# Kernel optimization log

Measured on AMD Instinct MI355X. Metric: run time of the kernel, lower is better.

The kernel has to match this reference:

```python
import jax, jax.numpy as jnp
import numpy as np

N_NODES, N_EDGES = 100000, 1600000
D_IN, D_H, D_OUT = 256, 128, 32


def _gcn_conv(x, W, b, row, col, norm, n):
    # GCNConv: transform, normalized gather from source nodes, scatter-sum at targets, bias.
    h = x @ W                                   # [n, d_out]
    msgs = h[row] * norm[:, None]               # [E', d_out] edge messages
    out = jax.ops.segment_sum(msgs, col, num_segments=n)
    return out + b


def setup_inputs() -> dict:
    key = jax.random.key(0)
    k = jax.random.split(key, 6)
    x = jax.random.normal(k[0], (N_NODES, D_IN), dtype=jnp.float32)
    edge_index = jax.random.randint(k[1], (2, N_EDGES), 0, N_NODES, dtype=jnp.int64)
    # Glorot-ish scaled params (GCNConv lin has no bias; bias added post-aggregation)
    W1 = jax.random.normal(k[2], (D_IN, D_H), dtype=jnp.float32) * (1.0 / np.sqrt(D_IN))
    b1 = jnp.zeros((D_H,), dtype=jnp.float32)
    W2 = jax.random.normal(k[3], (D_H, D_OUT), dtype=jnp.float32) * (1.0 / np.sqrt(D_H))
    b2 = jnp.zeros((D_OUT,), dtype=jnp.float32)
    return {"x": x, "W1": W1, "b1": b1, "W2": W2, "b2": b2, "edge_index": edge_index}


def reference(x, W1, b1, W2, b2, edge_index):
    n = x.shape[0]
    loops = jnp.arange(n, dtype=edge_index.dtype)
    row = jnp.concatenate([edge_index[0], loops])   # sources (incl. self-loops)
    col = jnp.concatenate([edge_index[1], loops])   # targets
    # symmetric normalization deg^{-1/2} (deg >= 1 because of self-loops)
    deg = jax.ops.segment_sum(jnp.ones_like(col, dtype=x.dtype), col, num_segments=n)
    dinv = deg ** -0.5
    norm = dinv[row] * dinv[col]
    h = jax.nn.relu(_gcn_conv(x, W1, b1, row, col, norm, n))
    # F.dropout(training=False) is identity in eval mode
    out = _gcn_conv(h, W2, b2, row, col, norm, n)
    return jax.nn.log_softmax(out, axis=1)
```

## Files before the change

kernel.cpp:

```cpp
#include <hip/hip_runtime.h>
#include <math.h>

#define N_NODES 100000
#define N_EDGES 1600000
#define D_IN 256
#define D_H 128
#define D_OUT 32
#define N_PAD 102400
#define NB 196
#define CAPB 10240
#define CHUNK 2048

typedef long long ll;
typedef unsigned int uint;
typedef unsigned short ushort;
typedef unsigned char uchar;
typedef short frag_ab __attribute__((ext_vector_type(8)));
typedef float frag_cd __attribute__((ext_vector_type(4)));

__device__ __forceinline__ ushort f2bf(float f) {
    uint u = __float_as_uint(f);
    u += 0x7FFFu + ((u >> 16) & 1u);
    return (ushort)(u >> 16);
}
__device__ __forceinline__ float bfl(uint u) { return __uint_as_float(u << 16); }
__device__ __forceinline__ float bfh(uint u) { return __uint_as_float(u & 0xFFFF0000u); }
__device__ __forceinline__ uint packbf(float a, float b) {
    return (uint)f2bf(a) | ((uint)f2bf(b) << 16);
}

__global__ __launch_bounds__(256) void k_bucketA(const int* __restrict__ row,
                                                 const int* __restrict__ col,
                                                 int* __restrict__ deg,
                                                 int* __restrict__ gcur,
                                                 uint* __restrict__ pairs,
                                                 const float* __restrict__ W1,
                                                 const float* __restrict__ W2,
                                                 ushort* __restrict__ w1t,
                                                 ushort* __restrict__ w2t, int e) {
    __shared__ int cnt[NB];
    __shared__ int lofs[NB];
    __shared__ int lstart[NB];
    __shared__ int sc[256];
    __shared__ uint spair[CHUNK];
    __shared__ uchar sbuck[CHUNK];
    const int t = threadIdx.x;
    for (int i = t; i < NB; i += 256) cnt[i] = 0;
    __syncthreads();
    const int base = blockIdx.x * CHUNK;
    const int end = min(base + CHUNK, e);
    const int valid = end - base;
    for (int idx = base + t; idx < end; idx += 256) {
        int c = col[idx];
        atomicAdd(&deg[c], 1);
        atomicAdd(&cnt[c >> 9], 1);
    }
    __syncthreads();
    int v = (t < NB) ? cnt[t] : 0;
    sc[t] = v;
    __syncthreads();
    for (int o = 1; o < 256; o <<= 1) {
        int u2 = (t >= o) ? sc[t - o] : 0;
        __syncthreads();
        sc[t] += u2;
        __syncthreads();
    }
    if (t < NB) {
        lofs[t] = sc[t] - v;
        lstart[t] = (v > 0) ? atomicAdd(&gcur[t], v) : 0;
        cnt[t] = 0;
    }
    __syncthreads();
    for (int idx = base + t; idx < end; idx += 256) {
        int c = col[idx], r = row[idx];
        int b = c >> 9;
        int pos = lofs[b] + atomicAdd(&cnt[b], 1);
        spair[pos] = ((uint)r << 9) | (uint)(c & 511);
        sbuck[pos] = (uchar)b;
    }
    __syncthreads();
    for (int i = t; i < valid; i += 256) {
        int b = sbuck[i];
        int rel = lstart[b] + (i - lofs[b]);
        if (rel < CAPB) pairs[b * CAPB + rel] = spair[i];
    }
    int gi = blockIdx.x * 256 + t;
    if (gi < D_IN * D_H) {
        int k = gi >> 7, nn = gi & 127;
        w1t[nn * D_IN + k] = f2bf(W1[gi]);
    } else if (gi < D_IN * D_H + D_H * D_OUT) {
        int j = gi - D_IN * D_H;
        int k = j >> 5, nn = j & 31;
        w2t[nn * D_H + k] = f2bf(W2[j]);
    }
}

__global__ __launch_bounds__(256) void k_fillB(const uint* __restrict__ pairs,
                                               const int* __restrict__ gcur,
                                               const int* __restrict__ deg,
                                               int* __restrict__ rp,
                                               float* __restrict__ dinv,
                                               int* __restrict__ csr_src, int n) {
    __shared__ int scsr[CAPB];
    __shared__ int lrp[512];
    __shared__ int cur[512];
    __shared__ int ssum[256];
    const int b = blockIdx.x, t = threadIdx.x;
    const int node0 = b << 9;
    int d0 = deg[node0 + 2 * t];
    int d1 = deg[node0 + 2 * t + 1];
    ssum[t] = d0 + d1;
    __syncthreads();
    for (int o = 1; o < 256; o <<= 1) {
        int u2 = (t >= o) ? ssum[t - o] : 0;
        __syncthreads();
        ssum[t] += u2;
        __syncthreads();
    }
    int excl = ssum[t] - (d0 + d1);
    lrp[2 * t] = excl;
    lrp[2 * t + 1] = excl + d0;
    cur[2 * t] = excl;
    cur[2 * t + 1] = excl + d0;
    __syncthreads();
    for (int i = t; i < 512; i += 256) {
        int vv = node0 + i;
        if (vv < n) {
            rp[vv] = b * CAPB + lrp[i];
            dinv[vv] = rsqrtf((float)(1 + deg[vv]));
        }
    }
    const int cnt = min(gcur[b], CAPB);
    const uint* pr = pairs + b * CAPB;
    for (int i = t; i < cnt; i += 256) {
        uint pp = pr[i];
        int pos = atomicAdd(&cur[pp & 511], 1);
        if (pos < CAPB) scsr[pos] = (int)(pp >> 9);
    }
    __syncthreads();
    for (int i = t; i < cnt; i += 256)
        csr_src[b * CAPB + i] = scsr[i];
}

__global__ __launch_bounds__(256, 3) void k_gemm1(const float* __restrict__ x,
                                                  const ushort* __restrict__ w1t,
                                                  const float* __restrict__ dinv,
                                                  ushort* __restrict__ hxs, int n) {
    const int tid = threadIdx.x;
    const int wv = tid >> 6, lane = tid & 63;
    const int lm = lane & 15, quad = lane >> 4;
    const int base = blockIdx.x * 128 + wv * 32;

    frag_cd acc[2][8];
#pragma unroll
    for (int mt = 0; mt < 2; mt++)
#pragma unroll
        for (int nt = 0; nt < 8; nt++) acc[mt][nt] = (frag_cd){0.f, 0.f, 0.f, 0.f};

    const float4* xr[2];
#pragma unroll
    for (int mt = 0; mt < 2; mt++) {
        int node = base + mt * 16 + lm;
        xr[mt] = (const float4*)(x + (ll)min(node, n - 1) * D_IN);
    }

#pragma unroll
    for (int ks = 0; ks < 8; ks++) {
        frag_ab a[2];
#pragma unroll
        for (int mt = 0; mt < 2; mt++) {
            float4 v0 = xr[mt][ks * 8 + quad * 2];
            float4 v1 = xr[mt][ks * 8 + quad * 2 + 1];
            uint* ap = (uint*)&a[mt];
            ap[0] = packbf(v0.x, v0.y);
            ap[1] = packbf(v0.z, v0.w);
            ap[2] = packbf(v1.x, v1.y);
            ap[3] = packbf(v1.z, v1.w);
        }
#pragma unroll
        for (int nt = 0; nt < 8; nt++) {
            frag_ab b = *(const frag_ab*)&w1t[(nt * 16 + lm) * D_IN + ks * 32 + quad * 8];
#pragma unroll
            for (int mt = 0; mt < 2; mt++)
                acc[mt][nt] = __builtin_amdgcn_mfma_f32_16x16x32_bf16(
                    a[mt], b, acc[mt][nt], 0, 0, 0);
        }
    }

#pragma unroll
    for (int mt = 0; mt < 2; mt++) {
#pragma unroll
        for (int r = 0; r < 4; r++) {
            int node = base + mt * 16 + quad * 4 + r;
            if (node < n) {
                float dv = dinv[node];
#pragma unroll
                for (int nt = 0; nt < 8; nt++)
                    hxs[(ll)node * D_H + nt * 16 + lm] = f2bf(acc[mt][nt][r] * dv);
            }
        }
    }
}

__global__ __launch_bounds__(256) void k_agg1(const uint* __restrict__ hxs,
                                              const int* __restrict__ csr_src,
                                              const int* __restrict__ rp,
                                              const int* __restrict__ deg,
                                              const float* __restrict__ dinv,
                                              const float* __restrict__ b1,
                                              uint* __restrict__ h, int n) {
    int v = blockIdx.x * 4 + (threadIdx.x >> 6);
    if (v >= n) return;
    int lane = threadIdx.x & 63;
    uint u = hxs[v * 64 + lane];
    float a0 = bfl(u), a1 = bfh(u);
    int s = rp[v], e = s + deg[v];
    int i = s;
    for (; i + 7 < e; i += 8) {
        int s0 = csr_src[i], s1 = csr_src[i + 1];
        int s2 = csr_src[i + 2], s3 = csr_src[i + 3];
        int s4 = csr_src[i + 4], s5 = csr_src[i + 5];
        int s6 = csr_src[i + 6], s7 = csr_src[i + 7];
        uint u0 = hxs[s0 * 64 + lane], u1 = hxs[s1 * 64 + lane];
        uint u2 = hxs[s2 * 64 + lane], u3 = hxs[s3 * 64 + lane];
        uint u4 = hxs[s4 * 64 + lane], u5 = hxs[s5 * 64 + lane];
        uint u6 = hxs[s6 * 64 + lane], u7 = hxs[s7 * 64 + lane];
        a0 += bfl(u0) + bfl(u1) + bfl(u2) + bfl(u3) + bfl(u4) + bfl(u5) + bfl(u6) + bfl(u7);
        a1 += bfh(u0) + bfh(u1) + bfh(u2) + bfh(u3) + bfh(u4) + bfh(u5) + bfh(u6) + bfh(u7);
    }
    for (; i + 1 < e; i += 2) {
        int s0 = csr_src[i], s1 = csr_src[i + 1];
        uint u0 = hxs[s0 * 64 + lane], u1 = hxs[s1 * 64 + lane];
        a0 += bfl(u0) + bfl(u1);
        a1 += bfh(u0) + bfh(u1);
    }
    if (i < e) {
        uint u0 = hxs[csr_src[i] * 64 + lane];
        a0 += bfl(u0);
        a1 += bfh(u0);
    }
    float dv = dinv[v];
    float2 bb = ((const float2*)b1)[lane];
    h[v * 64 + lane] = packbf(fmaxf(fmaf(dv, a0, bb.x), 0.f),
                              fmaxf(fmaf(dv, a1, bb.y), 0.f));
}

__global__ __launch_bounds__(256) void k_gemm2(const ushort* __restrict__ h,
                                               const ushort* __restrict__ w2t,
                                               const float* __restrict__ dinv,
                                               ushort* __restrict__ hx2s, int n) {
    const int tid = threadIdx.x;
    const int wv = tid >> 6, lane = tid & 63;
    const int lm = lane & 15, quad = lane >> 4;
    const int base = blockIdx.x * 128 + wv * 32;

    frag_cd acc[2][2];
#pragma unroll
    for (int mt = 0; mt < 2; mt++)
#pragma unroll
        for (int nt = 0; nt < 2; nt++) acc[mt][nt] = (frag_cd){0.f, 0.f, 0.f, 0.f};

    const ushort* hr[2];
#pragma unroll
    for (int mt = 0; mt < 2; mt++) {
        int node = base + mt * 16 + lm;
        hr[mt] = h + (ll)min(node, n - 1) * D_H;
    }

#pragma unroll
    for (int ks = 0; ks < 4; ks++) {
        frag_ab a[2], b[2];
#pragma unroll
        for (int mt = 0; mt < 2; mt++)
            a[mt] = *(const frag_ab*)&hr[mt][ks * 32 + quad * 8];
#pragma unroll
        for (int nt = 0; nt < 2; nt++)
            b[nt] = *(const frag_ab*)&w2t[(nt * 16 + lm) * D_H + ks * 32 + quad * 8];
#pragma unroll
        for (int mt = 0; mt < 2; mt++)
#pragma unroll
            for (int nt = 0; nt < 2; nt++)
                acc[mt][nt] = __builtin_amdgcn_mfma_f32_16x16x32_bf16(
                    a[mt], b[nt], acc[mt][nt], 0, 0, 0);
    }

#pragma unroll
    for (int mt = 0; mt < 2; mt++) {
#pragma unroll
        for (int r = 0; r < 4; r++) {
            int node = base + mt * 16 + quad * 4 + r;
            if (node < n) {
                float dv = dinv[node];
#pragma unroll
                for (int nt = 0; nt < 2; nt++)
                    hx2s[(ll)node * D_OUT + nt * 16 + lm] = f2bf(acc[mt][nt][r] * dv);
            }
        }
    }
}

__global__ __launch_bounds__(256) void k_agg2(const uint* __restrict__ hx2s,
                                              const int* __restrict__ csr_src,
                                              const int* __restrict__ rp,
                                              const int* __restrict__ deg,
                                              const float* __restrict__ dinv,
                                              const float* __restrict__ b2,
                                              float2* __restrict__ out, int n) {
    int v = blockIdx.x * 16 + (threadIdx.x >> 4);
    if (v >= n) return;
    int l16 = threadIdx.x & 15;
    uint u = hx2s[v * 16 + l16];
    float a0 = bfl(u), a1 = bfh(u);
    int s = rp[v], e = s + deg[v];
    int i = s;
    for (; i + 7 < e; i += 8) {
        int s0 = csr_src[i], s1 = csr_src[i + 1];
        int s2 = csr_src[i + 2], s3 = csr_src[i + 3];
        int s4 = csr_src[i + 4], s5 = csr_src[i + 5];
        int s6 = csr_src[i + 6], s7 = csr_src[i + 7];
        uint u0 = hx2s[s0 * 16 + l16], u1 = hx2s[s1 * 16 + l16];
        uint u2 = hx2s[s2 * 16 + l16], u3 = hx2s[s3 * 16 + l16];
        uint u4 = hx2s[s4 * 16 + l16], u5 = hx2s[s5 * 16 + l16];
        uint u6 = hx2s[s6 * 16 + l16], u7 = hx2s[s7 * 16 + l16];
        a0 += bfl(u0) + bfl(u1) + bfl(u2) + bfl(u3) + bfl(u4) + bfl(u5) + bfl(u6) + bfl(u7);
        a1 += bfh(u0) + bfh(u1) + bfh(u2) + bfh(u3) + bfh(u4) + bfh(u5) + bfh(u6) + bfh(u7);
    }
    for (; i + 1 < e; i += 2) {
        int s0 = csr_src[i], s1 = csr_src[i + 1];
        uint u0 = hx2s[s0 * 16 + l16], u1 = hx2s[s1 * 16 + l16];
        a0 += bfl(u0) + bfl(u1);
        a1 += bfh(u0) + bfh(u1);
    }
    if (i < e) {
        uint u0 = hx2s[csr_src[i] * 16 + l16];
        a0 += bfl(u0);
        a1 += bfh(u0);
    }
    float dv = dinv[v];
    float2 bb = ((const float2*)b2)[l16];
    float t0 = fmaf(dv, a0, bb.x), t1 = fmaf(dv, a1, bb.y);
    float mx = fmaxf(t0, t1);
#pragma unroll
    for (int m = 8; m >= 1; m >>= 1) mx = fmaxf(mx, __shfl_xor(mx, m));
    float sum = __expf(t0 - mx) + __expf(t1 - mx);
#pragma unroll
    for (int m = 8; m >= 1; m >>= 1) sum += __shfl_xor(sum, m);
    float lse = mx + __logf(sum);
    out[v * 16 + l16] = make_float2(t0 - lse, t1 - lse);
}

extern "C" void kernel_launch(void* const* d_in, const int* in_sizes, int n_in,
                              void* d_out, int out_size, void* d_ws, size_t ws_size,
                              hipStream_t stream) {
    const float* x  = (const float*)d_in[0];
    const float* W1 = (const float*)d_in[1];
    const float* b1 = (const float*)d_in[2];
    const float* W2 = (const float*)d_in[3];
    const float* b2 = (const float*)d_in[4];
    const int*   ei = (const int*)d_in[5];
    const int* row = ei;
    const int* col = ei + N_EDGES;

    int*    ws_i    = (int*)d_ws;
    int*    deg     = ws_i;
    int*    gcur    = ws_i + N_PAD;
    int*    rp      = ws_i + N_PAD + 256;
    float*  dinv    = (float*)(ws_i + 2 * N_PAD + 256);
    int*    csr_src = ws_i + 3 * N_PAD + 256;
    uint*   pairs   = (uint*)(csr_src + NB * CAPB);
    ushort* w1t     = (ushort*)(pairs + NB * CAPB);
    ushort* w2t     = w1t + D_IN * D_H;
    ushort* hxs     = w2t + D_H * D_OUT;
    ushort* h       = hxs + (ll)N_NODES * D_H;
    ushort* hx2s    = h + (ll)N_NODES * D_H;

    const int n = N_NODES, e = N_EDGES;

    hipMemsetAsync(deg, 0, (N_PAD + 256) * sizeof(int), stream);
    k_bucketA<<<(e + CHUNK - 1) / CHUNK, 256, 0, stream>>>(row, col, deg, gcur, pairs,
                                                           W1, W2, w1t, w2t, e);
    k_fillB<<<NB, 256, 0, stream>>>(pairs, gcur, deg, rp, dinv, csr_src, n);

    k_gemm1<<<(n + 127) / 128, 256, 0, stream>>>(x, w1t, dinv, hxs, n);
    k_agg1<<<(n + 3) / 4, 256, 0, stream>>>((const uint*)hxs, csr_src, rp, deg, dinv, b1,
                                            (uint*)h, n);
    k_gemm2<<<(n + 127) / 128, 256, 0, stream>>>(h, w2t, dinv, hx2s, n);
    k_agg2<<<(n + 15) / 16, 256, 0, stream>>>((const uint*)hx2s, csr_src, rp, deg, dinv, b2,
                                              (float2*)d_out, n);
}
```

Baseline: 398.6 us.

## Fuse edge bucketing with first GEMM and derive degrees from bucket histograms

Edge bucketing and the first dense transform now run in one launch, with odd and even blocks taking different roles, so the memory-bound scatter and the MFMA GEMM can overlap. Node degrees are no longer built with global atomics after a memset. Instead, k_fillB counts them from the per-bucket pairs in shared memory and writes them out itself. Because dinv is not ready when the GEMM runs, the source-side normalization moves into agg1 as a per-edge dinv gather and FMA, which adds extra scattered loads to the aggregation.

```diff
diff --git a/kernel.cpp b/kernel.cpp
--- a/kernel.cpp
+++ b/kernel.cpp
@@ -29,15 +29,31 @@
     return (uint)f2bf(a) | ((uint)f2bf(b) << 16);
 }
 
-__global__ __launch_bounds__(256) void k_bucketA(const int* __restrict__ row,
-                                                 const int* __restrict__ col,
-                                                 int* __restrict__ deg,
-                                                 int* __restrict__ gcur,
-                                                 uint* __restrict__ pairs,
-                                                 const float* __restrict__ W1,
-                                                 const float* __restrict__ W2,
-                                                 ushort* __restrict__ w1t,
-                                                 ushort* __restrict__ w2t, int e) {
+__global__ __launch_bounds__(256) void k_prep(const float* __restrict__ W1,
+                                              const float* __restrict__ W2,
+                                              ushort* __restrict__ w1t,
+                                              ushort* __restrict__ w2t,
+                                              int* __restrict__ gcur) {
+    int gi = blockIdx.x * 256 + threadIdx.x;
+    if (blockIdx.x == 0) gcur[threadIdx.x] = 0;
+    if (gi < D_IN * D_H) {
+        int k = gi >> 7, nn = gi & 127;
+        w1t[nn * D_IN + k] = f2bf(W1[gi]);
+    } else if (gi < D_IN * D_H + D_H * D_OUT) {
+        int j = gi - D_IN * D_H;
+        int k = j >> 5, nn = j & 31;
+        w2t[nn * D_H + k] = f2bf(W2[j]);
+    }
+}
+
+__global__ __launch_bounds__(256, 3) void k_fused(const int* __restrict__ row,
+                                                  const int* __restrict__ col,
+                                                  int* __restrict__ gcur,
+                                                  uint* __restrict__ pairs,
+                                                  const float* __restrict__ x,
+                                                  const ushort* __restrict__ w1t,
+                                                  ushort* __restrict__ hxs,
+                                                  int n, int e) {
     __shared__ int cnt[NB];
     __shared__ int lofs[NB];
     __shared__ int lstart[NB];
@@ -45,70 +61,134 @@
     __shared__ uint spair[CHUNK];
     __shared__ uchar sbuck[CHUNK];
     const int t = threadIdx.x;
-    for (int i = t; i < NB; i += 256) cnt[i] = 0;
-    __syncthreads();
-    const int base = blockIdx.x * CHUNK;
-    const int end = min(base + CHUNK, e);
-    const int valid = end - base;
-    for (int idx = base + t; idx < end; idx += 256) {
-        int c = col[idx];
-        atomicAdd(&deg[c], 1);
-        atomicAdd(&cnt[c >> 9], 1);
-    }
-    __syncthreads();
-    int v = (t < NB) ? cnt[t] : 0;
-    sc[t] = v;
-    __syncthreads();
-    for (int o = 1; o < 256; o <<= 1) {
-        int u2 = (t >= o) ? sc[t - o] : 0;
-        __syncthreads();
-        sc[t] += u2;
-        __syncthreads();
-    }
-    if (t < NB) {
-        lofs[t] = sc[t] - v;
-        lstart[t] = (v > 0) ? atomicAdd(&gcur[t], v) : 0;
-        cnt[t] = 0;
-    }
-    __syncthreads();
-    for (int idx = base + t; idx < end; idx += 256) {
-        int c = col[idx], r = row[idx];
-        int b = c >> 9;
-        int pos = lofs[b] + atomicAdd(&cnt[b], 1);
-        spair[pos] = ((uint)r << 9) | (uint)(c & 511);
-        sbuck[pos] = (uchar)b;
-    }
-    __syncthreads();
-    for (int i = t; i < valid; i += 256) {
-        int b = sbuck[i];
-        int rel = lstart[b] + (i - lofs[b]);
-        if (rel < CAPB) pairs[b * CAPB + rel] = spair[i];
-    }
-    int gi = blockIdx.x * 256 + t;
-    if (gi < D_IN * D_H) {
-        int k = gi >> 7, nn = gi & 127;
-        w1t[nn * D_IN + k] = f2bf(W1[gi]);
-    } else if (gi < D_IN * D_H + D_H * D_OUT) {
-        int j = gi - D_IN * D_H;
-        int k = j >> 5, nn = j & 31;
-        w2t[nn * D_H + k] = f2bf(W2[j]);
+    const int role = blockIdx.x & 1;
+    const int id = blockIdx.x >> 1;
+
+    if (role == 0) {
+        for (int i = t; i < NB; i += 256) cnt[i] = 0;
+        __syncthreads();
+        const int base = id * CHUNK;
+        const int end = min(base + CHUNK, e);
+        const int valid = end - base;
+        int rs[8], cs[8];
+#pragma unroll
+        for (int j = 0; j < 8; j++) {
+            int idx = base + t + j * 256;
+            bool ok = idx < end;
+            int c = ok ? col[idx] : 0;
+            rs[j] = ok ? row[idx] : 0;
+            cs[j] = ok ? c : -1;
+            if (ok) atomicAdd(&cnt[c >> 9], 1);
+        }
+        __syncthreads();
+        int v = (t < NB) ? cnt[t] : 0;
+        sc[t] = v;
+        __syncthreads();
+        for (int o = 1; o < 256; o <<= 1) {
+            int u2 = (t >= o) ? sc[t - o] : 0;
+            __syncthreads();
+            sc[t] += u2;
+            __syncthreads();
+        }
+        if (t < NB) {
+            lofs[t] = sc[t] - v;
+            lstart[t] = (v > 0) ? atomicAdd(&gcur[t], v) : 0;
+            cnt[t] = 0;
+        }
+        __syncthreads();
+#pragma unroll
+        for (int j = 0; j < 8; j++) {
+            int c = cs[j];
+            if (c >= 0) {
+                int b = c >> 9;
+                int pos = lofs[b] + atomicAdd(&cnt[b], 1);
+                spair[pos] = ((uint)rs[j] << 9) | (uint)(c & 511);
+                sbuck[pos] = (uchar)b;
+            }
+        }
+        __syncthreads();
+        for (int i = t; i < valid; i += 256) {
+            int b = sbuck[i];
+            int rel = lstart[b] + (i - lofs[b]);
+            if (rel < CAPB) pairs[b * CAPB + rel] = spair[i];
+        }
+    } else {
+        const int wv = t >> 6, lane = t & 63;
+        const int lm = lane & 15, quad = lane >> 4;
+        const int base = id * 128 + wv * 32;
+
+        frag_cd acc[2][8];
+#pragma unroll
+        for (int mt = 0; mt < 2; mt++)
+#pragma unroll
+            for (int nt = 0; nt < 8; nt++) acc[mt][nt] = (frag_cd){0.f, 0.f, 0.f, 0.f};
+
+        const float4* xr[2];
+#pragma unroll
+        for (int mt = 0; mt < 2; mt++) {
+            int node = base + mt * 16 + lm;
+            xr[mt] = (const float4*)(x + (ll)min(node, n - 1) * D_IN);
+        }
+
+#pragma unroll
+        for (int ks = 0; ks < 8; ks++) {
+            frag_ab a[2];
+#pragma unroll
+            for (int mt = 0; mt < 2; mt++) {
+                float4 v0 = xr[mt][ks * 8 + quad * 2];
+                float4 v1 = xr[mt][ks * 8 + quad * 2 + 1];
+                uint* ap = (uint*)&a[mt];
+                ap[0] = packbf(v0.x, v0.y);
+                ap[1] = packbf(v0.z, v0.w);
+                ap[2] = packbf(v1.x, v1.y);
+                ap[3] = packbf(v1.z, v1.w);
+            }
+#pragma unroll
+            for (int nt = 0; nt < 8; nt++) {
+                frag_ab b = *(const frag_ab*)&w1t[(nt * 16 + lm) * D_IN + ks * 32 + quad * 8];
+#pragma unroll
+                for (int mt = 0; mt < 2; mt++)
+                    acc[mt][nt] = __builtin_amdgcn_mfma_f32_16x16x32_bf16(
+                        a[mt], b, acc[mt][nt], 0, 0, 0);
+            }
+        }
+
+#pragma unroll
+        for (int mt = 0; mt < 2; mt++) {
+#pragma unroll
+            for (int r = 0; r < 4; r++) {
+                int node = base + mt * 16 + quad * 4 + r;
+                if (node < n) {
+#pragma unroll
+                    for (int nt = 0; nt < 8; nt++)
+                        hxs[(ll)node * D_H + nt * 16 + lm] = f2bf(acc[mt][nt][r]);
+                }
+            }
+        }
     }
 }
 
 __global__ __launch_bounds__(256) void k_fillB(const uint* __restrict__ pairs,
                                                const int* __restrict__ gcur,
-                                               const int* __restrict__ deg,
+                                               int* __restrict__ deg,
                                                int* __restrict__ rp,
                                                float* __restrict__ dinv,
                                                int* __restrict__ csr_src, int n) {
     __shared__ int scsr[CAPB];
+    __shared__ int hcnt[512];
     __shared__ int lrp[512];
     __shared__ int cur[512];
     __shared__ int ssum[256];
     const int b = blockIdx.x, t = threadIdx.x;
     const int node0 = b << 9;
-    int d0 = deg[node0 + 2 * t];
-    int d1 = deg[node0 + 2 * t + 1];
+    hcnt[t] = 0;
+    hcnt[t + 256] = 0;
+    __syncthreads();
+    const int cnt = min(gcur[b], CAPB);
+    const uint* pr = pairs + b * CAPB;
+    for (int i = t; i < cnt; i += 256) atomicAdd(&hcnt[pr[i] & 511], 1);
+    __syncthreads();
+    int d0 = hcnt[2 * t], d1 = hcnt[2 * t + 1];
     ssum[t] = d0 + d1;
     __syncthreads();
     for (int o = 1; o < 256; o <<= 1) {
@@ -127,11 +207,10 @@
         int vv = node0 + i;
         if (vv < n) {
             rp[vv] = b * CAPB + lrp[i];
-            dinv[vv] = rsqrtf((float)(1 + deg[vv]));
-        }
-    }
-    const int cnt = min(gcur[b], CAPB);
-    const uint* pr = pairs + b * CAPB;
+            deg[vv] = hcnt[i];
+            dinv[vv] = rsqrtf((float)(1 + hcnt[i]));
+        }
+    }
     for (int i = t; i < cnt; i += 256) {
         uint pp = pr[i];
         int pos = atomicAdd(&cur[pp & 511], 1);
@@ -140,66 +219,6 @@
     __syncthreads();
     for (int i = t; i < cnt; i += 256)
         csr_src[b * CAPB + i] = scsr[i];
-}
-
-__global__ __launch_bounds__(256, 3) void k_gemm1(const float* __restrict__ x,
-                                                  const ushort* __restrict__ w1t,
-                                                  const float* __restrict__ dinv,
-                                                  ushort* __restrict__ hxs, int n) {
-    const int tid = threadIdx.x;
-    const int wv = tid >> 6, lane = tid & 63;
-    const int lm = lane & 15, quad = lane >> 4;
-    const int base = blockIdx.x * 128 + wv * 32;
-
-    frag_cd acc[2][8];
-#pragma unroll
-    for (int mt = 0; mt < 2; mt++)
-#pragma unroll
-        for (int nt = 0; nt < 8; nt++) acc[mt][nt] = (frag_cd){0.f, 0.f, 0.f, 0.f};
-
-    const float4* xr[2];
-#pragma unroll
-    for (int mt = 0; mt < 2; mt++) {
-        int node = base + mt * 16 + lm;
-        xr[mt] = (const float4*)(x + (ll)min(node, n - 1) * D_IN);
-    }
-
-#pragma unroll
-    for (int ks = 0; ks < 8; ks++) {
-        frag_ab a[2];
-#pragma unroll
-        for (int mt = 0; mt < 2; mt++) {
-            float4 v0 = xr[mt][ks * 8 + quad * 2];
-            float4 v1 = xr[mt][ks * 8 + quad * 2 + 1];
-            uint* ap = (uint*)&a[mt];
-            ap[0] = packbf(v0.x, v0.y);
-            ap[1] = packbf(v0.z, v0.w);
-            ap[2] = packbf(v1.x, v1.y);
-            ap[3] = packbf(v1.z, v1.w);
-        }
-#pragma unroll
-        for (int nt = 0; nt < 8; nt++) {
-            frag_ab b = *(const frag_ab*)&w1t[(nt * 16 + lm) * D_IN + ks * 32 + quad * 8];
-#pragma unroll
-            for (int mt = 0; mt < 2; mt++)
-                acc[mt][nt] = __builtin_amdgcn_mfma_f32_16x16x32_bf16(
-                    a[mt], b, acc[mt][nt], 0, 0, 0);
-        }
-    }
-
-#pragma unroll
-    for (int mt = 0; mt < 2; mt++) {
-#pragma unroll
-        for (int r = 0; r < 4; r++) {
-            int node = base + mt * 16 + quad * 4 + r;
-            if (node < n) {
-                float dv = dinv[node];
-#pragma unroll
-                for (int nt = 0; nt < 8; nt++)
-                    hxs[(ll)node * D_H + nt * 16 + lm] = f2bf(acc[mt][nt][r] * dv);
-            }
-        }
-    }
 }
 
 __global__ __launch_bounds__(256) void k_agg1(const uint* __restrict__ hxs,
@@ -212,8 +231,9 @@
     int v = blockIdx.x * 4 + (threadIdx.x >> 6);
     if (v >= n) return;
     int lane = threadIdx.x & 63;
+    float dv = dinv[v];
     uint u = hxs[v * 64 + lane];
-    float a0 = bfl(u), a1 = bfh(u);
+    float a0 = dv * bfl(u), a1 = dv * bfh(u);
     int s = rp[v], e = s + deg[v];
     int i = s;
     for (; i + 7 < e; i += 8) {
@@ -221,25 +241,35 @@
         int s2 = csr_src[i + 2], s3 = csr_src[i + 3];
         int s4 = csr_src[i + 4], s5 = csr_src[i + 5];
         int s6 = csr_src[i + 6], s7 = csr_src[i + 7];
+        float n0 = dinv[s0], n1 = dinv[s1], n2 = dinv[s2], n3 = dinv[s3];
+        float n4 = dinv[s4], n5 = dinv[s5], n6 = dinv[s6], n7 = dinv[s7];
         uint u0 = hxs[s0 * 64 + lane], u1 = hxs[s1 * 64 + lane];
         uint u2 = hxs[s2 * 64 + lane], u3 = hxs[s3 * 64 + lane];
         uint u4 = hxs[s4 * 64 + lane], u5 = hxs[s5 * 64 + lane];
         uint u6 = hxs[s6 * 64 + lane], u7 = hxs[s7 * 64 + lane];
-        a0 += bfl(u0) + bfl(u1) + bfl(u2) + bfl(u3) + bfl(u4) + bfl(u5) + bfl(u6) + bfl(u7);
-        a1 += bfh(u0) + bfh(u1) + bfh(u2) + bfh(u3) + bfh(u4) + bfh(u5) + bfh(u6) + bfh(u7);
+        a0 = fmaf(n0, bfl(u0), a0); a0 = fmaf(n1, bfl(u1), a0);
+        a0 = fmaf(n2, bfl(u2), a0); a0 = fmaf(n3, bfl(u3), a0);
+        a0 = fmaf(n4, bfl(u4), a0); a0 = fmaf(n5, bfl(u5), a0);
+        a0 = fmaf(n6, bfl(u6), a0); a0 = fmaf(n7, bfl(u7), a0);
+        a1 = fmaf(n0, bfh(u0), a1); a1 = fmaf(n1, bfh(u1), a1);
+        a1 = fmaf(n2, bfh(u2), a1); a1 = fmaf(n3, bfh(u3), a1);
+        a1 = fmaf(n4, bfh(u4), a1); a1 = fmaf(n5, bfh(u5), a1);
+        a1 = fmaf(n6, bfh(u6), a1); a1 = fmaf(n7, bfh(u7), a1);
     }
     for (; i + 1 < e; i += 2) {
         int s0 = csr_src[i], s1 = csr_src[i + 1];
+        float n0 = dinv[s0], n1 = dinv[s1];
         uint u0 = hxs[s0 * 64 + lane], u1 = hxs[s1 * 64 + lane];
-        a0 += bfl(u0) + bfl(u1);
-        a1 += bfh(u0) + bfh(u1);
+        a0 = fmaf(n0, bfl(u0), a0); a0 = fmaf(n1, bfl(u1), a0);
+        a1 = fmaf(n0, bfh(u0), a1); a1 = fmaf(n1, bfh(u1), a1);
     }
     if (i < e) {
-        uint u0 = hxs[csr_src[i] * 64 + lane];
-        a0 += bfl(u0);
-        a1 += bfh(u0);
-    }
-    float dv = dinv[v];
+        int s0 = csr_src[i];
+        float n0 = dinv[s0];
+        uint u0 = hxs[s0 * 64 + lane];
+        a0 = fmaf(n0, bfl(u0), a0);
+        a1 = fmaf(n0, bfh(u0), a1);
+    }
     float2 bb = ((const float2*)b1)[lane];
     h[v * 64 + lane] = packbf(fmaxf(fmaf(dv, a0, bb.x), 0.f),
                               fmaxf(fmaf(dv, a1, bb.y), 0.f));
@@ -376,12 +406,13 @@
 
     const int n = N_NODES, e = N_EDGES;
 
-    hipMemsetAsync(deg, 0, (N_PAD + 256) * sizeof(int), stream);
-    k_bucketA<<<(e + CHUNK - 1) / CHUNK, 256, 0, stream>>>(row, col, deg, gcur, pairs,
-                                                           W1, W2, w1t, w2t, e);
+    k_prep<<<(D_IN * D_H + D_H * D_OUT + 255) / 256, 256, 0, stream>>>(W1, W2, w1t, w2t, gcur);
+
+    const int GA = (e + CHUNK - 1) / CHUNK;
+    const int GG = (n + 127) / 128;
+    k_fused<<<GA + GG, 256, 0, stream>>>(row, col, gcur, pairs, x, w1t, hxs, n, e);
+
     k_fillB<<<NB, 256, 0, stream>>>(pairs, gcur, deg, rp, dinv, csr_src, n);
-
-    k_gemm1<<<(n + 127) / 128, 256, 0, stream>>>(x, w1t, dinv, hxs, n);
     k_agg1<<<(n + 3) / 4, 256, 0, stream>>>((const uint*)hxs, csr_src, rp, deg, dinv, b1,
                                             (uint*)h, n);
     k_gemm2<<<(n + 127) / 128, 256, 0, stream>>>(h, w2t, dinv, hx2s, n);
```

New measurement: 371.1 us. 6.9% less time.
